# Performance work log

Measured on AMD Instinct MI355X. Metric: run time of the kernel, lower is better.

## Reference

```python
import jax, jax.numpy as jnp
import numpy as np

D_MODEL = 768
D_STATE = 16
D_CONV = 4
EXPAND = 2
D_INNER = EXPAND * D_MODEL          # 1536
DT_RANK = (D_MODEL + 15) // 16      # 48
HID = 4 * D_MODEL                   # 3072
B_SZ = 4
SEQ = 2048


def layer_norm(x, w, b, eps=1e-5):
    m = x.mean(-1, keepdims=True)
    v = jnp.mean((x - m) ** 2, axis=-1, keepdims=True)
    return (x - m) * jax.lax.rsqrt(v + eps) * w + b


def setup_inputs() -> dict:
    key = jax.random.key(0)
    ks = jax.random.split(key, 10)
    s = 0.02
    inp = {
        "x": jax.random.normal(ks[0], (B_SZ, SEQ, D_MODEL), jnp.float32),
        "ln1_w": jnp.ones((D_MODEL,), jnp.float32),
        "ln1_b": jnp.zeros((D_MODEL,), jnp.float32),
        "W_in": jax.random.normal(ks[1], (2 * D_INNER, D_MODEL), jnp.float32) * s,
        "conv_w": jax.random.normal(ks[2], (D_INNER, 1, D_CONV), jnp.float32) * s,
        "conv_b": jnp.zeros((D_INNER,), jnp.float32),
        "W_x": jax.random.normal(ks[3], (DT_RANK + 2 * D_STATE, D_INNER), jnp.float32) * s,
        "W_dt": jax.random.normal(ks[4], (D_INNER, DT_RANK), jnp.float32) * s,
        "b_dt": jax.random.normal(ks[5], (D_INNER,), jnp.float32) * 0.1,
        "A_log": jnp.log(jnp.broadcast_to(
            jnp.arange(1, D_STATE + 1, dtype=jnp.float32), (D_INNER, D_STATE))),
        "D_skip": jnp.ones((D_INNER,), jnp.float32),
        "W_out": jax.random.normal(ks[6], (D_MODEL, D_INNER), jnp.float32) * s,
        "ln2_w": jnp.ones((D_MODEL,), jnp.float32),
        "ln2_b": jnp.zeros((D_MODEL,), jnp.float32),
        "W1": jax.random.normal(ks[7], (HID, D_MODEL), jnp.float32) * s,
        "b1": jnp.zeros((HID,), jnp.float32),
        "W2": jax.random.normal(ks[8], (D_MODEL, HID), jnp.float32) * s,
        "b2": jnp.zeros((D_MODEL,), jnp.float32),
    }
    return inp


def mamba_mixer(x, W_in, conv_w, conv_b, W_x, W_dt, b_dt, A_log, D_skip, W_out):
    B, L, _ = x.shape
    xz = x @ W_in.T                       # (B, L, 2E)
    u, z = jnp.split(xz, 2, axis=-1)      # (B, L, E) each
    # causal depthwise conv1d over time
    u = jnp.transpose(u, (0, 2, 1))       # (B, E, L)
    u = jax.lax.conv_general_dilated(
        u, conv_w, window_strides=(1,), padding=[(D_CONV - 1, 0)],
        feature_group_count=D_INNER,
        dimension_numbers=("NCH", "OIH", "NCH")) + conv_b[None, :, None]
    u = jax.nn.silu(u)
    u = jnp.transpose(u, (0, 2, 1))       # (B, L, E)
    # input-dependent dt, B, C
    x_dbl = u @ W_x.T                     # (B, L, R + 2N)
    dt_r = x_dbl[..., :DT_RANK]
    Bm = x_dbl[..., DT_RANK:DT_RANK + D_STATE]
    Cm = x_dbl[..., DT_RANK + D_STATE:]
    dt = jax.nn.softplus(dt_r @ W_dt.T + b_dt)   # (B, L, E)
    A = -jnp.exp(A_log)                   # (E, N)

    def step(h, inp):
        dt_t, B_t, C_t, u_t = inp         # (B,E),(B,N),(B,N),(B,E)
        dA = jnp.exp(dt_t[:, :, None] * A)
        h = h * dA + (dt_t * u_t)[:, :, None] * B_t[:, None, :]
        y = jnp.einsum("ben,bn->be", h, C_t)
        return h, y

    xs = (jnp.transpose(dt, (1, 0, 2)), jnp.transpose(Bm, (1, 0, 2)),
          jnp.transpose(Cm, (1, 0, 2)), jnp.transpose(u, (1, 0, 2)))
    h0 = jnp.zeros((B, D_INNER, D_STATE), x.dtype)
    _, ys = jax.lax.scan(step, h0, xs)    # ys: (L, B, E)
    y = jnp.transpose(ys, (1, 0, 2)) + u * D_skip
    y = y * jax.nn.silu(z)
    return y @ W_out.T


def reference(x, ln1_w, ln1_b, W_in, conv_w, conv_b, W_x, W_dt, b_dt, A_log,
              D_skip, W_out, ln2_w, ln2_b, W1, b1, W2, b2):
    h = x + mamba_mixer(layer_norm(x, ln1_w, ln1_b),
                        W_in, conv_w, conv_b, W_x, W_dt, b_dt,
                        A_log, D_skip, W_out)
    m = layer_norm(h, ln2_w, ln2_b)
    m = jax.nn.relu(m @ W1.T + b1) @ W2.T + b2   # MLP(dim, 4*dim, dim, 2)
    return h + m
```

## Files before the change

kernel.cpp:

```cpp
#include <hip/hip_runtime.h>
#include <cstdint>

typedef __bf16 bf16;
typedef __bf16 bf16x8 __attribute__((ext_vector_type(8)));
typedef float  f32x4  __attribute__((ext_vector_type(4)));

#define NCH 32
#define CT  64

__device__ __forceinline__ void g2l16(const bf16* g, bf16* l) {
  __builtin_amdgcn_global_load_lds(
      (const __attribute__((address_space(1))) unsigned int*)g,
      (__attribute__((address_space(3))) unsigned int*)l, 16, 0, 0);
}

__global__ __launch_bounds__(256) void cast_pad(const float* __restrict__ src, bf16* __restrict__ dst,
                                                int cd, int rs, int cs) {
  int c = blockIdx.x * 256 + threadIdx.x;
  int r = blockIdx.y;
  if (c >= cd) return;
  float v = (r < rs && c < cs) ? src[(size_t)r * cs + c] : 0.f;
  dst[(size_t)r * cd + c] = (bf16)v;
}

__global__ __launch_bounds__(256) void ln_cast(const float* __restrict__ x, const float* __restrict__ w,
                                               const float* __restrict__ b, bf16* __restrict__ out) {
  const int row = blockIdx.x;
  const int tid = threadIdx.x;
  const float* xr = x + (size_t)row * 768;
  float v0 = xr[tid], v1 = xr[tid + 256], v2 = xr[tid + 512];
  float s = v0 + v1 + v2;
  __shared__ float red[8];
  #pragma unroll
  for (int o = 32; o; o >>= 1) s += __shfl_down(s, o);
  if ((tid & 63) == 0) red[tid >> 6] = s;
  __syncthreads();
  float mean = (red[0] + red[1] + red[2] + red[3]) * (1.f / 768.f);
  float d0 = v0 - mean, d1 = v1 - mean, d2 = v2 - mean;
  float q = d0 * d0 + d1 * d1 + d2 * d2;
  #pragma unroll
  for (int o = 32; o; o >>= 1) q += __shfl_down(q, o);
  if ((tid & 63) == 0) red[4 + (tid >> 6)] = q;
  __syncthreads();
  float var = (red[4] + red[5] + red[6] + red[7]) * (1.f / 768.f);
  float inv = rsqrtf(var + 1e-5f);
  bf16* orow = out + (size_t)row * 768;
  orow[tid]       = (bf16)(d0 * inv * w[tid]       + b[tid]);
  orow[tid + 256] = (bf16)(d1 * inv * w[tid + 256] + b[tid + 256]);
  orow[tid + 512] = (bf16)(d2 * inv * w[tid + 512] + b[tid + 512]);
}

__global__ __launch_bounds__(256) void conv_silu(const bf16* __restrict__ xz, const float* __restrict__ cw,
                                                 const float* __restrict__ cb, bf16* __restrict__ u) {
  int c = blockIdx.x * 256 + threadIdx.x;
  int r = blockIdx.y;
  int t = r & 2047;
  const float4 wv = ((const float4*)cw)[c];
  float acc = cb[c];
  const bf16* col = xz + c;
  if (t >= 3) {
    acc += (float)col[(size_t)(r - 3) * 3072] * wv.x;
    acc += (float)col[(size_t)(r - 2) * 3072] * wv.y;
    acc += (float)col[(size_t)(r - 1) * 3072] * wv.z;
  } else {
    if (t >= 2) acc += (float)col[(size_t)(r - 2) * 3072] * wv.y;
    if (t >= 1) acc += (float)col[(size_t)(r - 1) * 3072] * wv.z;
  }
  acc += (float)col[(size_t)r * 3072] * wv.w;
  float sg = 1.f / (1.f + __expf(-acc));
  u[(size_t)r * 1536 + c] = (bf16)(acc * sg);
}

template<int EPI>
__global__ __launch_bounds__(256) void gemm_bt(
    const bf16* __restrict__ A, const bf16* __restrict__ B,
    int N, int K, int lda, int ldb,
    void* __restrict__ C0, void* __restrict__ C1,
    const float* __restrict__ aux, const float* __restrict__ aux2)
{
  __shared__ alignas(16) bf16 As[2][4096];
  __shared__ alignas(16) bf16 Bs[2][4096];
  const int tid = threadIdx.x;
  const int w = tid >> 6, l = tid & 63;

  const int nwg = gridDim.x * gridDim.y;
  const int orig = blockIdx.x + gridDim.x * blockIdx.y;
  const int n8 = nwg >> 3;
  const int sw = (orig & 7) * n8 + (orig >> 3);
  const int m0 = (sw / gridDim.x) * 128;
  const int n0 = (sw % gridDim.x) * 128;

  const int wr = (w >> 1) * 64, wc = (w & 1) * 64;

  const int srow = tid >> 2;
  const int slot = tid & 3;
  const int scol = (slot ^ (srow & 3)) * 8;
  const bf16* ag  = A + (size_t)(m0 + srow) * lda + scol;
  const bf16* ag2 = A + (size_t)(m0 + 64 + srow) * lda + scol;
  const bf16* bg  = B + (size_t)(n0 + srow) * ldb + scol;
  const bf16* bg2 = B + (size_t)(n0 + 64 + srow) * ldb + scol;

  f32x4 acc[4][4] = {};
  const int fr = l & 15, kb = (l >> 4) * 8;

  g2l16(ag,  &As[0][w * 512]);
  g2l16(ag2, &As[0][2048 + w * 512]);
  g2l16(bg,  &Bs[0][w * 512]);
  g2l16(bg2, &Bs[0][2048 + w * 512]);
  __syncthreads();

  int cur = 0;
  for (int k0 = 0; k0 < K; k0 += 32) {
    if (k0 + 32 < K) {
      int nx = cur ^ 1, kn = k0 + 32;
      g2l16(ag  + kn, &As[nx][w * 512]);
      g2l16(ag2 + kn, &As[nx][2048 + w * 512]);
      g2l16(bg  + kn, &Bs[nx][w * 512]);
      g2l16(bg2 + kn, &Bs[nx][2048 + w * 512]);
    }
    bf16x8 af[4], bfr[4];
    #pragma unroll
    for (int i = 0; i < 4; ++i) {
      const int ra = wr + i * 16 + fr;
      const int rb = wc + i * 16 + fr;
      af[i]  = *(const bf16x8*)&As[cur][ra * 32 + (kb ^ ((ra & 3) << 3))];
      bfr[i] = *(const bf16x8*)&Bs[cur][rb * 32 + (kb ^ ((rb & 3) << 3))];
    }
    #pragma unroll
    for (int i = 0; i < 4; ++i)
      #pragma unroll
      for (int j = 0; j < 4; ++j)
        acc[i][j] = __builtin_amdgcn_mfma_f32_16x16x32_bf16(af[i], bfr[j], acc[i][j], 0, 0, 0);
    __syncthreads();
    cur ^= 1;
  }

  const int fq = (l >> 4) * 4;
  #pragma unroll
  for (int i = 0; i < 4; ++i) {
    #pragma unroll
    for (int j = 0; j < 4; ++j) {
      int row = m0 + wr + i * 16 + fq;
      int col = n0 + wc + j * 16 + fr;
      f32x4 v = acc[i][j];
      #pragma unroll
      for (int jj = 0; jj < 4; ++jj) {
        size_t idx = (size_t)(row + jj) * N + col;
        float val = v[jj];
        if constexpr (EPI == 0) {
          ((bf16*)C0)[idx] = (bf16)val;
        } else if constexpr (EPI == 1) {
          ((float*)C0)[idx] = val;
          ((bf16*)C1)[idx] = (bf16)val;
        } else if constexpr (EPI == 2) {
          float xv = val + aux[col];
          float sp = (xv > 20.f) ? xv : log1pf(__expf(xv));
          ((bf16*)C0)[idx] = (bf16)sp;
        } else if constexpr (EPI == 3) {
          ((float*)C0)[idx] = val + aux2[idx];
        } else if constexpr (EPI == 4) {
          float xv = val + aux[col];
          ((bf16*)C0)[idx] = (bf16)(xv > 0.f ? xv : 0.f);
        } else if constexpr (EPI == 5) {
          ((float*)C0)[idx] = val + aux[col] + aux2[idx];
        }
      }
    }
  }
}

__global__ __launch_bounds__(256) void scan_pass1(
    const bf16* __restrict__ dtb, const bf16* __restrict__ ub,
    const float* __restrict__ xdbl, const float* __restrict__ A_log,
    float* __restrict__ Pp, float* __restrict__ hend)
{
  __shared__ float Bs[CT * 16];
  const int tid = threadIdx.x;
  const int cg = blockIdx.x, k = blockIdx.y, b = blockIdx.z;
  const int c = cg * 256 + tid;
  const size_t rowbase = (size_t)b * 2048 + (size_t)k * CT;

  for (int i = tid; i < CT * 16; i += 256) {
    int tr = i >> 4, q = i & 15;
    Bs[i] = xdbl[(rowbase + tr) * 128 + 48 + q];
  }
  float al2[16];
  {
    const float4* ap = (const float4*)&A_log[c * 16];
    #pragma unroll
    for (int qq = 0; qq < 4; ++qq) {
      float4 a = ap[qq];
      al2[qq*4+0] = -__expf(a.x) * 1.44269504f;
      al2[qq*4+1] = -__expf(a.y) * 1.44269504f;
      al2[qq*4+2] = -__expf(a.z) * 1.44269504f;
      al2[qq*4+3] = -__expf(a.w) * 1.44269504f;
    }
  }
  __syncthreads();

  float h[16];
  #pragma unroll
  for (int n = 0; n < 16; ++n) h[n] = 0.f;
  float sdt = 0.f;

  for (int t8 = 0; t8 < CT / 8; ++t8) {
    float dv[8], xv[8];
    #pragma unroll
    for (int tt = 0; tt < 8; ++tt) {
      size_t row = rowbase + t8 * 8 + tt;
      float d = (float)dtb[row * 1536 + c];
      dv[tt] = d;
      xv[tt] = d * (float)ub[row * 1536 + c];
    }
    #pragma unroll
    for (int tt = 0; tt < 8; ++tt) {
      float d = dv[tt], x = xv[tt];
      sdt += d;
      float Bv[16];
      const float4* bp = (const float4*)&Bs[(t8 * 8 + tt) * 16];
      ((float4*)Bv)[0] = bp[0]; ((float4*)Bv)[1] = bp[1];
      ((float4*)Bv)[2] = bp[2]; ((float4*)Bv)[3] = bp[3];
      #pragma unroll
      for (int n = 0; n < 16; ++n) {
        float e = exp2f(d * al2[n]);
        h[n] = h[n] * e + x * Bv[n];
      }
    }
  }
  size_t off = ((size_t)(b * NCH + k) * 1536 + c) * 16;
  float P[16];
  #pragma unroll
  for (int n = 0; n < 16; ++n) P[n] = exp2f(al2[n] * sdt);
  #pragma unroll
  for (int qq = 0; qq < 4; ++qq) {
    ((float4*)&Pp[off])[qq]   = ((float4*)P)[qq];
    ((float4*)&hend[off])[qq] = ((float4*)h)[qq];
  }
}

__global__ __launch_bounds__(256) void scan_pass2(
    const float* __restrict__ Pp, const float* __restrict__ hend, float* __restrict__ hstart)
{
  int t = blockIdx.x * 256 + threadIdx.x;
  int b = t / 24576;
  int r = t - b * 24576;
  size_t base = (size_t)b * (NCH * 24576) + r;
  float hs = 0.f;
  for (int k = 0; k < NCH; ++k) {
    size_t off = base + (size_t)k * 24576;
    hstart[off] = hs;
    hs = Pp[off] * hs + hend[off];
  }
}

__global__ __launch_bounds__(256) void scan_pass3(
    const bf16* __restrict__ dtb, const bf16* __restrict__ ub, const bf16* __restrict__ xzb,
    const float* __restrict__ xdbl, const float* __restrict__ A_log, const float* __restrict__ Dskip,
    const float* __restrict__ hstart, bf16* __restrict__ yg)
{
  __shared__ float BCs[CT * 32];
  const int tid = threadIdx.x;
  const int cg = blockIdx.x, k = blockIdx.y, b = blockIdx.z;
  const int c = cg * 256 + tid;
  const size_t rowbase = (size_t)b * 2048 + (size_t)k * CT;

  for (int i = tid; i < CT * 32; i += 256) {
    int tr = i >> 5, q = i & 31;
    BCs[i] = xdbl[(rowbase + tr) * 128 + 48 + q];
  }
  float al2[16];
  {
    const float4* ap = (const float4*)&A_log[c * 16];
    #pragma unroll
    for (int qq = 0; qq < 4; ++qq) {
      float4 a = ap[qq];
      al2[qq*4+0] = -__expf(a.x) * 1.44269504f;
      al2[qq*4+1] = -__expf(a.y) * 1.44269504f;
      al2[qq*4+2] = -__expf(a.z) * 1.44269504f;
      al2[qq*4+3] = -__expf(a.w) * 1.44269504f;
    }
  }
  const float dsk = Dskip[c];
  float h[16];
  {
    size_t off = ((size_t)(b * NCH + k) * 1536 + c) * 16;
    #pragma unroll
    for (int qq = 0; qq < 4; ++qq) ((float4*)h)[qq] = ((const float4*)&hstart[off])[qq];
  }
  __syncthreads();

  for (int t8 = 0; t8 < CT / 8; ++t8) {
    float dv[8], uv[8], gv[8];
    #pragma unroll
    for (int tt = 0; tt < 8; ++tt) {
      size_t row = rowbase + t8 * 8 + tt;
      dv[tt] = (float)dtb[row * 1536 + c];
      uv[tt] = (float)ub[row * 1536 + c];
      float zv = (float)xzb[row * 3072 + 1536 + c];
      gv[tt] = zv / (1.f + __expf(-zv));
    }
    #pragma unroll
    for (int tt = 0; tt < 8; ++tt) {
      float d = dv[tt], x = d * uv[tt];
      float BC[32];
      const float4* bp = (const float4*)&BCs[(t8 * 8 + tt) * 32];
      #pragma unroll
      for (int qq = 0; qq < 8; ++qq) ((float4*)BC)[qq] = bp[qq];
      float y = 0.f;
      #pragma unroll
      for (int n = 0; n < 16; ++n) {
        float e = exp2f(d * al2[n]);
        h[n] = h[n] * e + x * BC[n];
        y += h[n] * BC[16 + n];
      }
      size_t row = rowbase + t8 * 8 + tt;
      yg[row * 1536 + c] = (bf16)((y + uv[tt] * dsk) * gv[tt]);
    }
  }
}

extern "C" void kernel_launch(void* const* d_in, const int* in_sizes, int n_in,
                              void* d_out, int out_size, void* d_ws, size_t ws_size,
                              hipStream_t stream) {
  const float* x     = (const float*)d_in[0];
  const float* ln1w  = (const float*)d_in[1];
  const float* ln1b  = (const float*)d_in[2];
  const float* W_in  = (const float*)d_in[3];
  const float* convw = (const float*)d_in[4];
  const float* convb = (const float*)d_in[5];
  const float* W_x   = (const float*)d_in[6];
  const float* W_dt  = (const float*)d_in[7];
  const float* b_dt  = (const float*)d_in[8];
  const float* A_log = (const float*)d_in[9];
  const float* Dskip = (const float*)d_in[10];
  const float* W_out = (const float*)d_in[11];
  const float* ln2w  = (const float*)d_in[12];
  const float* ln2b  = (const float*)d_in[13];
  const float* W1    = (const float*)d_in[14];
  const float* b1    = (const float*)d_in[15];
  const float* W2    = (const float*)d_in[16];
  const float* b2    = (const float*)d_in[17];
  float* out = (float*)d_out;

  uint8_t* ws = (uint8_t*)d_ws;
  size_t off = 0;
  auto alloc = [&](size_t bytes) { void* p = ws + off; off = (off + bytes + 255) & ~(size_t)255; return p; };

  bf16*  wInb  = (bf16*)alloc(3072ull * 768 * 2);
  bf16*  wXb   = (bf16*)alloc(128ull * 1536 * 2);
  bf16*  wDtb  = (bf16*)alloc(1536ull * 64 * 2);
  bf16*  wOutb = (bf16*)alloc(768ull * 1536 * 2);
  bf16*  w1b   = (bf16*)alloc(3072ull * 768 * 2);
  bf16*  w2b   = (bf16*)alloc(768ull * 3072 * 2);
  bf16*  xln   = (bf16*)alloc(8192ull * 768 * 2);
  bf16*  xz    = (bf16*)alloc(8192ull * 3072 * 2);
  bf16*  u     = (bf16*)alloc(8192ull * 1536 * 2);
  float* xdblf = (float*)alloc(8192ull * 128 * 4);
  bf16*  xdblb = (bf16*)alloc(8192ull * 128 * 2);
  bf16*  dtb   = (bf16*)alloc(8192ull * 1536 * 2);
  bf16*  ygate = (bf16*)alloc(8192ull * 1536 * 2);
  float* hbuf  = (float*)alloc(8192ull * 768 * 4);
  float* hendb = (float*)alloc(4ull * NCH * 1536 * 16 * 4);
  (void)ws_size; (void)in_sizes; (void)n_in; (void)out_size;

  float* Pbuf    = (float*)xln;
  float* hstartb = (float*)hbuf;

  cast_pad<<<dim3(3, 3072),  256, 0, stream>>>(W_in,  wInb,  768,  3072, 768);
  cast_pad<<<dim3(6, 128),   256, 0, stream>>>(W_x,   wXb,   1536, 80,   1536);
  cast_pad<<<dim3(1, 1536),  256, 0, stream>>>(W_dt,  wDtb,  64,   1536, 48);
  cast_pad<<<dim3(6, 768),   256, 0, stream>>>(W_out, wOutb, 1536, 768,  1536);
  cast_pad<<<dim3(3, 3072),  256, 0, stream>>>(W1,    w1b,   768,  3072, 768);
  cast_pad<<<dim3(12, 768),  256, 0, stream>>>(W2,    w2b,   3072, 768,  3072);

  ln_cast<<<8192, 256, 0, stream>>>(x, ln1w, ln1b, xln);

  gemm_bt<0><<<dim3(24, 64), 256, 0, stream>>>(xln, wInb, 3072, 768, 768, 768, xz, nullptr, nullptr, nullptr);
  conv_silu<<<dim3(6, 8192), 256, 0, stream>>>(xz, convw, convb, u);
  gemm_bt<1><<<dim3(1, 64), 256, 0, stream>>>(u, wXb, 128, 1536, 1536, 1536, xdblf, xdblb, nullptr, nullptr);
  gemm_bt<2><<<dim3(12, 64), 256, 0, stream>>>(xdblb, wDtb, 1536, 64, 128, 64, dtb, nullptr, b_dt, nullptr);
  scan_pass1<<<dim3(6, NCH, 4), 256, 0, stream>>>(dtb, u, xdblf, A_log, Pbuf, hendb);
  scan_pass2<<<384, 256, 0, stream>>>(Pbuf, hendb, hstartb);
  scan_pass3<<<dim3(6, NCH, 4), 256, 0, stream>>>(dtb, u, xz, xdblf, A_log, Dskip, hstartb, ygate);
  gemm_bt<3><<<dim3(6, 64), 256, 0, stream>>>(ygate, wOutb, 768, 1536, 1536, 1536, hbuf, nullptr, nullptr, x);
  ln_cast<<<8192, 256, 0, stream>>>(hbuf, ln2w, ln2b, xln);
  gemm_bt<4><<<dim3(24, 64), 256, 0, stream>>>(xln, w1b, 3072, 768, 768, 768, xz, nullptr, b1, nullptr);
  gemm_bt<5><<<dim3(6, 64), 256, 0, stream>>>(xz, w2b, 768, 3072, 3072, 3072, out, nullptr, b2, hbuf);
}
```

Baseline: 652.7 us.

## Transpose scan inputs to channel-major and precompute gate for vectorized scan loads

The dt GEMM epilogue now writes dt and a copy of u in a channel-major (transposed) layout. A new kernel computes silu(z) and stores it transposed, so the scan passes can load 8 consecutive timesteps per thread with one vector load instead of strided scalar loads. The chunk count is doubled and the chunk length halved for more scan parallelism. In exchange there are extra transpose writes and a new kernel launch, and stores from the GEMM epilogue and transpose kernel may be poorly coalesced. The scan buffers now reuse the xz and u workspaces.

New measurement: 847.8 us. +29.9%, slower.

```diff
diff --git a/kernel.cpp b/kernel.cpp
--- a/kernel.cpp
+++ b/kernel.cpp
@@ -2,11 +2,12 @@
 #include <cstdint>
 
 typedef __bf16 bf16;
+typedef __bf16 bf16x4 __attribute__((ext_vector_type(4)));
 typedef __bf16 bf16x8 __attribute__((ext_vector_type(8)));
 typedef float  f32x4  __attribute__((ext_vector_type(4)));
 
-#define NCH 32
-#define CT  64
+#define NCH 64
+#define CT  32
 
 __device__ __forceinline__ void g2l16(const bf16* g, bf16* l) {
   __builtin_amdgcn_global_load_lds(
@@ -71,12 +72,32 @@
   u[(size_t)r * 1536 + c] = (bf16)(acc * sg);
 }
 
+__global__ __launch_bounds__(256) void zt_silu(const bf16* __restrict__ xz, bf16* __restrict__ gT) {
+  __shared__ float zs[64][65];
+  const int t0 = blockIdx.x * 64;
+  const int c0 = blockIdx.y * 64;
+  const int lx = threadIdx.x & 63, ly = threadIdx.x >> 6;
+  #pragma unroll
+  for (int k = 0; k < 16; ++k) {
+    int t = ly + k * 4;
+    float z = (float)xz[(size_t)(t0 + t) * 3072 + 1536 + c0 + lx];
+    zs[t][lx] = z / (1.f + __expf(-z));
+  }
+  __syncthreads();
+  #pragma unroll
+  for (int k = 0; k < 16; ++k) {
+    int c = ly + k * 4;
+    gT[(size_t)(c0 + c) * 8192 + t0 + lx] = (bf16)zs[lx][c];
+  }
+}
+
 template<int EPI>
 __global__ __launch_bounds__(256) void gemm_bt(
     const bf16* __restrict__ A, const bf16* __restrict__ B,
     int N, int K, int lda, int ldb,
     void* __restrict__ C0, void* __restrict__ C1,
-    const float* __restrict__ aux, const float* __restrict__ aux2)
+    const float* __restrict__ aux, const float* __restrict__ aux2,
+    const bf16* __restrict__ uin)
 {
   __shared__ alignas(16) bf16 As[2][4096];
   __shared__ alignas(16) bf16 Bs[2][4096];
@@ -143,26 +164,35 @@
       int row = m0 + wr + i * 16 + fq;
       int col = n0 + wc + j * 16 + fr;
       f32x4 v = acc[i][j];
-      #pragma unroll
-      for (int jj = 0; jj < 4; ++jj) {
-        size_t idx = (size_t)(row + jj) * N + col;
-        float val = v[jj];
-        if constexpr (EPI == 0) {
-          ((bf16*)C0)[idx] = (bf16)val;
-        } else if constexpr (EPI == 1) {
-          ((float*)C0)[idx] = val;
-          ((bf16*)C1)[idx] = (bf16)val;
-        } else if constexpr (EPI == 2) {
-          float xv = val + aux[col];
+      if constexpr (EPI == 2) {
+        bf16x4 dq, uq;
+        #pragma unroll
+        for (int jj = 0; jj < 4; ++jj) {
+          float xv = v[jj] + aux[col];
           float sp = (xv > 20.f) ? xv : log1pf(__expf(xv));
-          ((bf16*)C0)[idx] = (bf16)sp;
-        } else if constexpr (EPI == 3) {
-          ((float*)C0)[idx] = val + aux2[idx];
-        } else if constexpr (EPI == 4) {
-          float xv = val + aux[col];
-          ((bf16*)C0)[idx] = (bf16)(xv > 0.f ? xv : 0.f);
-        } else if constexpr (EPI == 5) {
-          ((float*)C0)[idx] = val + aux[col] + aux2[idx];
+          dq[jj] = (bf16)sp;
+          uq[jj] = uin[(size_t)(row + jj) * 1536 + col];
+        }
+        *(bf16x4*)((bf16*)C0 + (size_t)col * 8192 + row) = dq;
+        *(bf16x4*)((bf16*)C1 + (size_t)col * 8192 + row) = uq;
+      } else {
+        #pragma unroll
+        for (int jj = 0; jj < 4; ++jj) {
+          size_t idx = (size_t)(row + jj) * N + col;
+          float val = v[jj];
+          if constexpr (EPI == 0) {
+            ((bf16*)C0)[idx] = (bf16)val;
+          } else if constexpr (EPI == 1) {
+            ((float*)C0)[idx] = val;
+            ((bf16*)C1)[idx] = (bf16)val;
+          } else if constexpr (EPI == 3) {
+            ((float*)C0)[idx] = val + aux2[idx];
+          } else if constexpr (EPI == 4) {
+            float xv = val + aux[col];
+            ((bf16*)C0)[idx] = (bf16)(xv > 0.f ? xv : 0.f);
+          } else if constexpr (EPI == 5) {
+            ((float*)C0)[idx] = val + aux[col] + aux2[idx];
+          }
         }
       }
     }
@@ -170,7 +200,7 @@
 }
 
 __global__ __launch_bounds__(256) void scan_pass1(
-    const bf16* __restrict__ dtb, const bf16* __restrict__ ub,
+    const bf16* __restrict__ dtT, const bf16* __restrict__ uT,
     const float* __restrict__ xdbl, const float* __restrict__ A_log,
     float* __restrict__ Pp, float* __restrict__ hend)
 {
@@ -203,18 +233,15 @@
   for (int n = 0; n < 16; ++n) h[n] = 0.f;
   float sdt = 0.f;
 
+  const bf16* dp = dtT + (size_t)c * 8192 + rowbase;
+  const bf16* up = uT  + (size_t)c * 8192 + rowbase;
   for (int t8 = 0; t8 < CT / 8; ++t8) {
-    float dv[8], xv[8];
+    bf16x8 d8 = *(const bf16x8*)(dp + t8 * 8);
+    bf16x8 u8 = *(const bf16x8*)(up + t8 * 8);
     #pragma unroll
     for (int tt = 0; tt < 8; ++tt) {
-      size_t row = rowbase + t8 * 8 + tt;
-      float d = (float)dtb[row * 1536 + c];
-      dv[tt] = d;
-      xv[tt] = d * (float)ub[row * 1536 + c];
-    }
-    #pragma unroll
-    for (int tt = 0; tt < 8; ++tt) {
-      float d = dv[tt], x = xv[tt];
+      float d = (float)d8[tt];
+      float x = d * (float)u8[tt];
       sdt += d;
       float Bv[16];
       const float4* bp = (const float4*)&Bs[(t8 * 8 + tt) * 16];
@@ -254,7 +281,7 @@
 }
 
 __global__ __launch_bounds__(256) void scan_pass3(
-    const bf16* __restrict__ dtb, const bf16* __restrict__ ub, const bf16* __restrict__ xzb,
+    const bf16* __restrict__ dtT, const bf16* __restrict__ uT, const bf16* __restrict__ gT,
     const float* __restrict__ xdbl, const float* __restrict__ A_log, const float* __restrict__ Dskip,
     const float* __restrict__ hstart, bf16* __restrict__ yg)
 {
@@ -289,19 +316,18 @@
   }
   __syncthreads();
 
+  const bf16* dp = dtT + (size_t)c * 8192 + rowbase;
+  const bf16* up = uT  + (size_t)c * 8192 + rowbase;
+  const bf16* gp = gT  + (size_t)c * 8192 + rowbase;
   for (int t8 = 0; t8 < CT / 8; ++t8) {
-    float dv[8], uv[8], gv[8];
+    bf16x8 d8 = *(const bf16x8*)(dp + t8 * 8);
+    bf16x8 u8 = *(const bf16x8*)(up + t8 * 8);
+    bf16x8 g8 = *(const bf16x8*)(gp + t8 * 8);
     #pragma unroll
     for (int tt = 0; tt < 8; ++tt) {
-      size_t row = rowbase + t8 * 8 + tt;
-      dv[tt] = (float)dtb[row * 1536 + c];
-      uv[tt] = (float)ub[row * 1536 + c];
-      float zv = (float)xzb[row * 3072 + 1536 + c];
-      gv[tt] = zv / (1.f + __expf(-zv));
-    }
-    #pragma unroll
-    for (int tt = 0; tt < 8; ++tt) {
-      float d = dv[tt], x = d * uv[tt];
+      float d = (float)d8[tt];
+      float uv = (float)u8[tt];
+      float x = d * uv;
       float BC[32];
       const float4* bp = (const float4*)&BCs[(t8 * 8 + tt) * 32];
       #pragma unroll
@@ -313,8 +339,7 @@
         h[n] = h[n] * e + x * BC[n];
         y += h[n] * BC[16 + n];
       }
-      size_t row = rowbase + t8 * 8 + tt;
-      yg[row * 1536 + c] = (bf16)((y + uv[tt] * dsk) * gv[tt]);
+      yg[(rowbase + t8 * 8 + tt) * 1536 + c] = (bf16)((y + uv * dsk) * (float)g8[tt]);
     }
   }
 }
@@ -357,13 +382,15 @@
   bf16*  u     = (bf16*)alloc(8192ull * 1536 * 2);
   float* xdblf = (float*)alloc(8192ull * 128 * 4);
   bf16*  xdblb = (bf16*)alloc(8192ull * 128 * 2);
-  bf16*  dtb   = (bf16*)alloc(8192ull * 1536 * 2);
   bf16*  ygate = (bf16*)alloc(8192ull * 1536 * 2);
   float* hbuf  = (float*)alloc(8192ull * 768 * 4);
-  float* hendb = (float*)alloc(4ull * NCH * 1536 * 16 * 4);
+  bf16*  dtT   = (bf16*)alloc(1536ull * 8192 * 2);
+  bf16*  uTb   = (bf16*)alloc(1536ull * 8192 * 2);
+  bf16*  gT    = (bf16*)alloc(1536ull * 8192 * 2);
   (void)ws_size; (void)in_sizes; (void)n_in; (void)out_size;
 
-  float* Pbuf    = (float*)xln;
+  float* Pbuf    = (float*)xz;
+  float* hendb   = (float*)u;
   float* hstartb = (float*)hbuf;
 
   cast_pad<<<dim3(3, 3072),  256, 0, stream>>>(W_in,  wInb,  768,  3072, 768);
@@ -375,15 +402,16 @@
 
   ln_cast<<<8192, 256, 0, stream>>>(x, ln1w, ln1b, xln);
 
-  gemm_bt<0><<<dim3(24, 64), 256, 0, stream>>>(xln, wInb, 3072, 768, 768, 768, xz, nullptr, nullptr, nullptr);
+  gemm_bt<0><<<dim3(24, 64), 256, 0, stream>>>(xln, wInb, 3072, 768, 768, 768, xz, nullptr, nullptr, nullptr, nullptr);
   conv_silu<<<dim3(6, 8192), 256, 0, stream>>>(xz, convw, convb, u);
-  gemm_bt<1><<<dim3(1, 64), 256, 0, stream>>>(u, wXb, 128, 1536, 1536, 1536, xdblf, xdblb, nullptr, nullptr);
-  gemm_bt<2><<<dim3(12, 64), 256, 0, stream>>>(xdblb, wDtb, 1536, 64, 128, 64, dtb, nullptr, b_dt, nullptr);
-  scan_pass1<<<dim3(6, NCH, 4), 256, 0, stream>>>(dtb, u, xdblf, A_log, Pbuf, hendb);
+  gemm_bt<1><<<dim3(1, 64), 256, 0, stream>>>(u, wXb, 128, 1536, 1536, 1536, xdblf, xdblb, nullptr, nullptr, nullptr);
+  gemm_bt<2><<<dim3(12, 64), 256, 0, stream>>>(xdblb, wDtb, 1536, 64, 128, 64, dtT, uTb, b_dt, nullptr, u);
+  zt_silu<<<dim3(128, 24), 256, 0, stream>>>(xz, gT);
+  scan_pass1<<<dim3(6, NCH, 4), 256, 0, stream>>>(dtT, uTb, xdblf, A_log, Pbuf, hendb);
   scan_pass2<<<384, 256, 0, stream>>>(Pbuf, hendb, hstartb);
-  scan_pass3<<<dim3(6, NCH, 4), 256, 0, stream>>>(dtb, u, xz, xdblf, A_log, Dskip, hstartb, ygate);
-  gemm_bt<3><<<dim3(6, 64), 256, 0, stream>>>(ygate, wOutb, 768, 1536, 1536, 1536, hbuf, nullptr, nullptr, x);
+  scan_pass3<<<dim3(6, NCH, 4), 256, 0, stream>>>(dtT, uTb, gT, xdblf, A_log, Dskip, hstartb, ygate);
+  gemm_bt<3><<<dim3(6, 64), 256, 0, stream>>>(ygate, wOutb, 768, 1536, 1536, 1536, hbuf, nullptr, nullptr, x, nullptr);
   ln_cast<<<8192, 256, 0, stream>>>(hbuf, ln2w, ln2b, xln);
-  gemm_bt<4><<<dim3(24, 64), 256, 0, stream>>>(xln, w1b, 3072, 768, 768, 768, xz, nullptr, b1, nullptr);
-  gemm_bt<5><<<dim3(6, 64), 256, 0, stream>>>(xz, w2b, 768, 3072, 3072, 3072, out, nullptr, b2, hbuf);
-}
+  gemm_bt<4><<<dim3(24, 64), 256, 0, stream>>>(xln, w1b, 3072, 768, 768, 768, xz, nullptr, b1, nullptr, nullptr);
+  gemm_bt<5><<<dim3(6, 64), 256, 0, stream>>>(xz, w2b, 768, 3072, 3072, 3072, out, nullptr, b2, hbuf, nullptr);
+}
```
